# Kernel optimization log

Measured on AMD Instinct MI355X. Metric: run time of the kernel, lower is better.

## Reference

```python
import jax, jax.numpy as jnp
import numpy as np

VOCAB, E, HID, T = 100000, 256, 512, 12
H = HID // 2          # per-direction LSTM hidden
B, S = 64, 256
START, STOP = 10, 11  # tag_to_ix['<START>'], tag_to_ix['<STOP>']
NEG = -10000.0


def setup_inputs() -> dict:
    key = jax.random.key(0)
    ks = jax.random.split(key, 16)
    inp = {
        'batch_sentence': jax.random.randint(ks[0], (B, S), 0, VOCAB),
        'sentence_length': S,
        'batch_chars2': jnp.zeros((1,), jnp.int64 if jax.config.jax_enable_x64 else jnp.int32),
        'chars2_length': 1,
        'emb': jax.random.normal(ks[1], (VOCAB, E), jnp.float32),
        # PyTorch LSTM layout: W_ih [4H, in], W_hh [4H, H], gate order i,f,g,o
        'Wih_f': jax.random.normal(ks[2], (4 * H, E), jnp.float32) * 0.05,
        'Whh_f': jax.random.normal(ks[3], (4 * H, H), jnp.float32) * 0.05,
        'bih_f': jnp.zeros((4 * H,), jnp.float32),
        'bhh_f': jnp.zeros((4 * H,), jnp.float32),
        'Wih_b': jax.random.normal(ks[4], (4 * H, E), jnp.float32) * 0.05,
        'Whh_b': jax.random.normal(ks[5], (4 * H, H), jnp.float32) * 0.05,
        'bih_b': jnp.zeros((4 * H,), jnp.float32),
        'bhh_b': jnp.zeros((4 * H,), jnp.float32),
        'Wt': jax.random.normal(ks[6], (T, HID), jnp.float32) * 0.05,
        'bt': jnp.zeros((T,), jnp.float32),
        'transitions': jax.random.normal(ks[7], (T, T), jnp.float32),
        # init_hidden() draws randn hidden state: h0/c0 [2 dirs, B, H]
        'h0': jax.random.normal(ks[8], (2, B, H), jnp.float32),
        'c0': jax.random.normal(ks[9], (2, B, H), jnp.float32),
    }
    return inp


def _lstm(x, h0, c0, Wih, Whh, bih, bhh):
    # x: [S, B, E] -> hs: [S, B, H]
    def step(carry, xt):
        h, c = carry
        g = xt @ Wih.T + h @ Whh.T + (bih + bhh)
        i, f, gg, o = jnp.split(g, 4, axis=-1)
        c = jax.nn.sigmoid(f) * c + jax.nn.sigmoid(i) * jnp.tanh(gg)
        h = jax.nn.sigmoid(o) * jnp.tanh(c)
        return (h, c), h
    _, hs = jax.lax.scan(step, (h0, c0), x)
    return hs


def _viterbi(feats, transitions):
    # feats: [S, T] emissions for one sequence
    init = jnp.full((T,), NEG, feats.dtype).at[START].set(0.0)

    def step(fv, feat):
        scores = fv[None, :] + transitions            # [next_tag, prev_tag]
        new_fv = jnp.max(scores, axis=1) + feat       # best prev per next
        bptr = jnp.argmax(scores, axis=1)
        return new_fv, bptr

    fv, bptrs = jax.lax.scan(step, init, feats)       # bptrs: [S, T]
    term = fv + transitions[STOP]
    term = term.at[STOP].set(NEG).at[START].set(NEG)  # torch code masks these
    last = jnp.argmax(term)
    score = term[last]

    def back(tag, bptr):
        return bptr[tag], tag                          # y_t = tag at time t
    _, path = jax.lax.scan(back, last, bptrs, reverse=True)
    return score, path


def reference(batch_sentence, sentence_length, batch_chars2, chars2_length,
              emb, Wih_f, Whh_f, bih_f, bhh_f, Wih_b, Whh_b, bih_b, bhh_b,
              Wt, bt, transitions, h0, c0):
    # word embeddings (dropout = identity at inference)
    x = emb[batch_sentence].transpose(1, 0, 2)        # [S, B, E]
    hf = _lstm(x, h0[0], c0[0], Wih_f, Whh_f, bih_f, bhh_f)
    hb = _lstm(x[::-1], h0[1], c0[1], Wih_b, Whh_b, bih_b, bhh_b)[::-1]
    out = jnp.concatenate([hf, hb], axis=-1)          # [S, B, HID]
    feats = out @ Wt.T + bt                           # [S, B, T]
    feats = feats.transpose(1, 0, 2)                  # [B, S, T]
    scores, paths = jax.vmap(_viterbi, in_axes=(0, None))(feats, transitions)
    return scores, paths
```

## Files before the change

kernel.cpp:

```cpp
#include <hip/hip_runtime.h>
#include <cstdint>
#include <cstddef>

#define EDIM 256
#define HID  512
#define NTAG 12
#define HDIM 256
#define BB   64
#define SS   256
#define START_TAG 10
#define STOP_TAG  11
#define NEGV (-10000.0f)
#define NWGD 32
#define UPW  8

typedef __attribute__((ext_vector_type(8))) short bf16x8;
typedef __attribute__((ext_vector_type(4))) float f32x4;

__device__ __forceinline__ unsigned short bf16_rne(float x) {
  union { float f; unsigned u; } a; a.f = x;
  return (unsigned short)((a.u + 0x7fffu + ((a.u >> 16) & 1u)) >> 16);
}
__device__ __forceinline__ float bf16_tof(unsigned short h) {
  union { unsigned u; float f; } a; a.u = ((unsigned)h) << 16; return a.f;
}
__device__ __forceinline__ void unpack8(const unsigned* u, bf16x8& hi, bf16x8& lo) {
#pragma unroll
  for (int j = 0; j < 8; ++j) {
    hi[j] = (short)(u[j] & 0xffffu);
    lo[j] = (short)(u[j] >> 16);
  }
}
__device__ __forceinline__ void pack_hilo(const float* xf, bf16x8& hi, bf16x8& lo) {
#pragma unroll
  for (int j = 0; j < 8; ++j) {
    unsigned short hb = bf16_rne(xf[j]);
    hi[j] = (short)hb;
    lo[j] = (short)bf16_rne(xf[j] - bf16_tof(hb));
  }
}

__global__ void k0_gather(const int* __restrict__ sent,
                          const float* __restrict__ emb,
                          unsigned int* __restrict__ xpk) {
  int t = blockIdx.x;
  for (int n = threadIdx.x; n < BB * EDIM; n += 256) {
    int b = n >> 8, k = n & 255;
    int tok = sent[b * SS + t];
    float x = emb[(size_t)tok * EDIM + k];
    unsigned short hb = bf16_rne(x);
    unsigned short lb = bf16_rne(x - bf16_tof(hb));
    xpk[((size_t)t * BB + b) * EDIM + k] = (unsigned)hb | ((unsigned)lb << 16);
  }
}

__global__ void __launch_bounds__(256)
k1_mfma(const unsigned int* __restrict__ xpk,
        const float* __restrict__ WihF, const float* __restrict__ WihB,
        const float* __restrict__ bihF, const float* __restrict__ bhhF,
        const float* __restrict__ bihB, const float* __restrict__ bhhB,
        float* __restrict__ pre) {
  int blk = blockIdx.x;
  int rg = blk & 15, t = (blk >> 4) & 255, d = blk >> 12;
  const float* Wih = d ? WihB : WihF;
  const float* bi  = d ? bihB : bihF;
  const float* bh2 = d ? bhhB : bhhF;
  int tid = threadIdx.x, lane = tid & 63, v = tid >> 6;
  int l15 = lane & 15, l4 = lane >> 4;

  int Rrow = rg * 64 + v * 16 + l15;
  const float* wrow = Wih + (size_t)Rrow * EDIM;
  bf16x8 Ahi[8], Alo[8];
#pragma unroll
  for (int kk = 0; kk < 8; ++kk) {
    float4 f0 = *(const float4*)(wrow + kk * 32 + l4 * 8);
    float4 f1 = *(const float4*)(wrow + kk * 32 + l4 * 8 + 4);
    float xf[8] = {f0.x, f0.y, f0.z, f0.w, f1.x, f1.y, f1.z, f1.w};
    pack_hilo(xf, Ahi[kk], Alo[kk]);
  }
  float b4[4];
#pragma unroll
  for (int r = 0; r < 4; ++r) {
    int Racc = rg * 64 + v * 16 + l4 * 4 + r;
    b4[r] = bi[Racc] + bh2[Racc];
  }
  const unsigned int* xt = xpk + (size_t)t * BB * EDIM;
  size_t obase = ((size_t)d * SS + t) * 1024 * BB;
#pragma unroll
  for (int ct = 0; ct < 4; ++ct) {
    f32x4 acc = {b4[0], b4[1], b4[2], b4[3]};
    int col = ct * 16 + l15;
    const unsigned int* xc = xt + (size_t)col * EDIM;
#pragma unroll
    for (int kk = 0; kk < 8; ++kk) {
      uint4 q0 = *(const uint4*)(xc + kk * 32 + l4 * 8);
      uint4 q1 = *(const uint4*)(xc + kk * 32 + l4 * 8 + 4);
      unsigned u[8] = {q0.x, q0.y, q0.z, q0.w, q1.x, q1.y, q1.z, q1.w};
      bf16x8 bhf, blf;
      unpack8(u, bhf, blf);
      acc = __builtin_amdgcn_mfma_f32_16x16x32_bf16(Ahi[kk], bhf, acc, 0, 0, 0);
      acc = __builtin_amdgcn_mfma_f32_16x16x32_bf16(Ahi[kk], blf, acc, 0, 0, 0);
      acc = __builtin_amdgcn_mfma_f32_16x16x32_bf16(Alo[kk], bhf, acc, 0, 0, 0);
    }
#pragma unroll
    for (int r = 0; r < 4; ++r) {
      int Racc = rg * 64 + v * 16 + l4 * 4 + r;
      pre[obase + (size_t)Racc * BB + col] = acc[r];
    }
  }
}

__global__ void __launch_bounds__(256, 1)
lstm_mfma(const float* __restrict__ WhhF, const float* __restrict__ WhhB,
          const float* __restrict__ h0, const float* __restrict__ c0,
          const float* __restrict__ pre, float* __restrict__ hseq,
          unsigned int* __restrict__ hx) {
  const int bid = blockIdx.x;
  const int d = bid >> 5, w = bid & 31;
  const int tid = threadIdx.x;
  const int lane = tid & 63;
  const int v = tid >> 6;
  const int l15 = lane & 15, l4 = lane >> 4;
  const int up = tid >> 5;
  const int b2 = (tid & 31) * 2;
  const float* Whh = d ? WhhB : WhhF;

  __shared__ float Cl[32][65];
  __shared__ float cst[UPW][BB];

  bf16x8 Ahi[2][8], Alo[2][8];
#pragma unroll
  for (int rt = 0; rt < 2; ++rt) {
    int i = rt * 16 + l15;
    int R = ((i >> 3) << 8) + w * UPW + (i & 7);
    const float* wrow = Whh + (size_t)R * HDIM;
#pragma unroll
    for (int kk = 0; kk < 8; ++kk) {
      float4 f0 = *(const float4*)(wrow + kk * 32 + l4 * 8);
      float4 f1 = *(const float4*)(wrow + kk * 32 + l4 * 8 + 4);
      float xf[8] = {f0.x, f0.y, f0.z, f0.w, f1.x, f1.y, f1.z, f1.w};
      pack_hilo(xf, Ahi[rt][kk], Alo[rt][kk]);
    }
  }
  cst[up][b2]     = c0[((size_t)d * BB + b2)     * HDIM + (w * UPW + up)];
  cst[up][b2 + 1] = c0[((size_t)d * BB + b2 + 1) * HDIM + (w * UPW + up)];
  __syncthreads();

  const int bcol = v * 16 + l15;
  const int kg = w * UPW + up;

  for (int s = 0; s < SS; ++s) {
    const int t = d ? (SS - 1 - s) : s;

    const float* pbase = pre + (((size_t)d * SS + t) * 1024) * BB + bcol;
    f32x4 acc0, acc1;
#pragma unroll
    for (int r = 0; r < 4; ++r) {
      int i0 = l4 * 4 + r;
      int R0 = ((i0 >> 3) << 8) + w * UPW + (i0 & 7);
      acc0[r] = pbase[(size_t)R0 * BB];
      int i1 = 16 + i0;
      int R1 = ((i1 >> 3) << 8) + w * UPW + (i1 & 7);
      acc1[r] = pbase[(size_t)R1 * BB];
    }

    unsigned uv[64];
    if (s > 0) {
      const unsigned* slot =
          hx + (((size_t)d * 4 + ((s - 1) & 3)) * HDIM) * BB + bcol;
      while (true) {
        int bad = 0;
#pragma unroll
        for (int kk = 0; kk < 8; ++kk)
#pragma unroll
          for (int j = 0; j < 8; ++j) {
            unsigned val = __hip_atomic_load(
                slot + (size_t)(kk * 32 + l4 * 8 + j) * BB,
                __ATOMIC_RELAXED, __HIP_MEMORY_SCOPE_AGENT);
            uv[kk * 8 + j] = val;
            bad |= (val == 0xFFFFFFFFu);
          }
        if (!__any(bad)) break;
        __builtin_amdgcn_s_sleep(1);
      }
      __builtin_amdgcn_sched_barrier(0);
    }

    {
      unsigned long long* ra = (unsigned long long*)(
          hx + (((size_t)d * 4 + ((s + 1) & 3)) * HDIM + kg) * BB + b2);
      __hip_atomic_store(ra, 0xFFFFFFFFFFFFFFFFull,
                         __ATOMIC_RELAXED, __HIP_MEMORY_SCOPE_AGENT);
    }

    if (s == 0) {
      const float* hrow = h0 + ((size_t)d * BB + bcol) * HDIM;
#pragma unroll
      for (int kk = 0; kk < 8; ++kk) {
        float4 f0 = *(const float4*)(hrow + kk * 32 + l4 * 8);
        float4 f1 = *(const float4*)(hrow + kk * 32 + l4 * 8 + 4);
        float xf[8] = {f0.x, f0.y, f0.z, f0.w, f1.x, f1.y, f1.z, f1.w};
        bf16x8 bh, bl;
        pack_hilo(xf, bh, bl);
        acc0 = __builtin_amdgcn_mfma_f32_16x16x32_bf16(Ahi[0][kk], bh, acc0, 0, 0, 0);
        acc0 = __builtin_amdgcn_mfma_f32_16x16x32_bf16(Ahi[0][kk], bl, acc0, 0, 0, 0);
        acc0 = __builtin_amdgcn_mfma_f32_16x16x32_bf16(Alo[0][kk], bh, acc0, 0, 0, 0);
        acc1 = __builtin_amdgcn_mfma_f32_16x16x32_bf16(Ahi[1][kk], bh, acc1, 0, 0, 0);
        acc1 = __builtin_amdgcn_mfma_f32_16x16x32_bf16(Ahi[1][kk], bl, acc1, 0, 0, 0);
        acc1 = __builtin_amdgcn_mfma_f32_16x16x32_bf16(Alo[1][kk], bh, acc1, 0, 0, 0);
      }
    } else {
#pragma unroll
      for (int kk = 0; kk < 8; ++kk) {
        bf16x8 bh, bl;
        unpack8(&uv[kk * 8], bh, bl);
        acc0 = __builtin_amdgcn_mfma_f32_16x16x32_bf16(Ahi[0][kk], bh, acc0, 0, 0, 0);
        acc0 = __builtin_amdgcn_mfma_f32_16x16x32_bf16(Ahi[0][kk], bl, acc0, 0, 0, 0);
        acc0 = __builtin_amdgcn_mfma_f32_16x16x32_bf16(Alo[0][kk], bh, acc0, 0, 0, 0);
        acc1 = __builtin_amdgcn_mfma_f32_16x16x32_bf16(Ahi[1][kk], bh, acc1, 0, 0, 0);
        acc1 = __builtin_amdgcn_mfma_f32_16x16x32_bf16(Ahi[1][kk], bl, acc1, 0, 0, 0);
        acc1 = __builtin_amdgcn_mfma_f32_16x16x32_bf16(Alo[1][kk], bh, acc1, 0, 0, 0);
      }
    }

#pragma unroll
    for (int r = 0; r < 4; ++r) {
      Cl[l4 * 4 + r][bcol] = acc0[r];
      Cl[16 + l4 * 4 + r][bcol] = acc1[r];
    }
    __syncthreads();

    float hn[2]; unsigned pv[2];
#pragma unroll
    for (int e = 0; e < 2; ++e) {
      int b = b2 + e;
      float iv = Cl[up][b], fv = Cl[8 + up][b];
      float gv = Cl[16 + up][b], ov = Cl[24 + up][b];
      float si = 1.f / (1.f + expf(-iv));
      float sf = 1.f / (1.f + expf(-fv));
      float so = 1.f / (1.f + expf(-ov));
      float cn = sf * cst[up][b] + si * tanhf(gv);
      cst[up][b] = cn;
      float h = so * tanhf(cn);
      hn[e] = h;
      unsigned short hb = bf16_rne(h);
      unsigned short lb = bf16_rne(h - bf16_tof(hb));
      pv[e] = (unsigned)hb | ((unsigned)lb << 16);
    }
    *(float2*)&hseq[(((size_t)d * SS + t) * HDIM + kg) * BB + b2] =
        make_float2(hn[0], hn[1]);

    asm volatile("s_waitcnt vmcnt(0)" ::: "memory");

    unsigned long long pv64 =
        (unsigned long long)pv[0] | ((unsigned long long)pv[1] << 32);
    unsigned long long* pd = (unsigned long long*)(
        hx + (((size_t)d * 4 + (s & 3)) * HDIM + kg) * BB + b2);
    __hip_atomic_store(pd, pv64, __ATOMIC_RELAXED, __HIP_MEMORY_SCOPE_AGENT);
  }
}

__global__ void k3_feats(const float* __restrict__ hseq,
                         const float* __restrict__ Wt,
                         const float* __restrict__ bt,
                         float* __restrict__ feats) {
  int t = blockIdx.x, tid = threadIdx.x;
  __shared__ float Wl[NTAG][HID];
  for (int n = tid; n < NTAG * HID; n += 256) Wl[n >> 9][n & 511] = Wt[n];
  __syncthreads();
  int b = tid & 63, tq = tid >> 6;
  float acc[3];
  for (int c = 0; c < 3; ++c) acc[c] = bt[tq * 3 + c];
  const float* hf = hseq + ((size_t)0 * SS + t) * HDIM * BB;
  const float* hb = hseq + ((size_t)1 * SS + t) * HDIM * BB;
  for (int k = 0; k < HDIM; ++k) {
    float h1 = hf[(size_t)k * BB + b];
    float h2 = hb[(size_t)k * BB + b];
#pragma unroll
    for (int c = 0; c < 3; ++c) {
      acc[c] += h1 * Wl[tq * 3 + c][k];
      acc[c] += h2 * Wl[tq * 3 + c][HDIM + k];
    }
  }
  for (int c = 0; c < 3; ++c)
    feats[((size_t)t * BB + b) * NTAG + tq * 3 + c] = acc[c];
}

__global__ void k4_viterbi(const float* __restrict__ feats,
                           const float* __restrict__ trans,
                           float* __restrict__ out) {
  int b = blockIdx.x, lane = threadIdx.x;
  __shared__ float tr[NTAG][NTAG];
  __shared__ float fv[NTAG], fnew[NTAG], term[NTAG];
  __shared__ unsigned char bp[SS][NTAG];
  for (int n = lane; n < NTAG * NTAG; n += 64) tr[n / NTAG][n % NTAG] = trans[n];
  if (lane < NTAG) fv[lane] = (lane == START_TAG) ? 0.f : NEGV;
  __syncthreads();
  for (int s = 0; s < SS; ++s) {
    if (lane < NTAG) {
      float best = fv[0] + tr[lane][0]; int arg = 0;
#pragma unroll
      for (int j = 1; j < NTAG; ++j) {
        float vv = fv[j] + tr[lane][j];
        if (vv > best) { best = vv; arg = j; }
      }
      fnew[lane] = best + feats[((size_t)s * BB + b) * NTAG + lane];
      bp[s][lane] = (unsigned char)arg;
    }
    __syncthreads();
    if (lane < NTAG) fv[lane] = fnew[lane];
    __syncthreads();
  }
  if (lane < NTAG) {
    float vv = fv[lane] + tr[STOP_TAG][lane];
    if (lane == STOP_TAG || lane == START_TAG) vv = NEGV;
    term[lane] = vv;
  }
  __syncthreads();
  if (lane == 0) {
    float best = term[0]; int arg = 0;
    for (int j = 1; j < NTAG; ++j)
      if (term[j] > best) { best = term[j]; arg = j; }
    out[b] = best;
    int cur = arg;
    for (int s = SS - 1; s >= 0; --s) {
      out[64 + (size_t)b * SS + s] = (float)cur;
      cur = bp[s][cur];
    }
  }
}

extern "C" void kernel_launch(void* const* d_in, const int* in_sizes, int n_in,
                              void* d_out, int out_size, void* d_ws, size_t ws_size,
                              hipStream_t stream) {
  (void)in_sizes; (void)n_in; (void)out_size;
  const int*   sent  = (const int*)d_in[0];
  const float* emb   = (const float*)d_in[4];
  const float* WihF  = (const float*)d_in[5];
  const float* WhhF  = (const float*)d_in[6];
  const float* bihF  = (const float*)d_in[7];
  const float* bhhF  = (const float*)d_in[8];
  const float* WihB  = (const float*)d_in[9];
  const float* WhhB  = (const float*)d_in[10];
  const float* bihB  = (const float*)d_in[11];
  const float* bhhB  = (const float*)d_in[12];
  const float* Wt    = (const float*)d_in[13];
  const float* bt    = (const float*)d_in[14];
  const float* trans = (const float*)d_in[15];
  const float* h0    = (const float*)d_in[16];
  const float* c0    = (const float*)d_in[17];
  float* out = (float*)d_out;

  char* ws = (char*)d_ws;
  unsigned int* hx = (unsigned int*)ws;
  float* pre   = (float*)(ws + 524288ull);
  float* hseq  = (float*)(ws + 524288ull + 134217728ull);
  unsigned int* xpk = (unsigned int*)hseq;
  float* feats = (float*)(ws + 524288ull + 134217728ull + 33554432ull);
  if (ws_size < 169082880ull) return;

  hipMemsetAsync(hx, 0xFF, 524288ull, stream);
  k0_gather<<<SS, 256, 0, stream>>>(sent, emb, xpk);
  k1_mfma<<<8192, 256, 0, stream>>>(xpk, WihF, WihB, bihF, bhhF, bihB, bhhB, pre);
  lstm_mfma<<<64, 256, 0, stream>>>(WhhF, WhhB, h0, c0, pre, hseq, hx);
  k3_feats<<<SS, 256, 0, stream>>>(hseq, Wt, bt, feats);
  k4_viterbi<<<BB, 64, 0, stream>>>(feats, trans, out);
}
```

Before: 1.597 ms.

## Remove LDS barrier from LSTM step via lane shuffles and 64-bit h exchange

The recurrent LSTM kernel no longer stages gate pre-activations through shared memory with a __syncthreads each step. Each lane now gets its four gates from its MFMA accumulators plus a cross-half __shfl_xor, and the cell state lives in registers. The hidden-state exchange buffer is relaid out batch-major, so each lane polls with 64-bit atomic loads (32 instead of 64). The three split-precision MFMA chains now use separate accumulators to shorten dependency chains. The hseq store moves after the publish store. Risks are the correctness of the new gate-to-lane mapping and less coalesced hseq writes.

```diff
diff --git a/kernel.cpp b/kernel.cpp
--- a/kernel.cpp
+++ b/kernel.cpp
@@ -11,7 +11,6 @@
 #define START_TAG 10
 #define STOP_TAG  11
 #define NEGV (-10000.0f)
-#define NWGD 32
 #define UPW  8
 
 typedef __attribute__((ext_vector_type(8))) short bf16x8;
@@ -114,19 +113,18 @@
 lstm_mfma(const float* __restrict__ WhhF, const float* __restrict__ WhhB,
           const float* __restrict__ h0, const float* __restrict__ c0,
           const float* __restrict__ pre, float* __restrict__ hseq,
-          unsigned int* __restrict__ hx) {
+          unsigned long long* __restrict__ hx64) {
   const int bid = blockIdx.x;
   const int d = bid >> 5, w = bid & 31;
   const int tid = threadIdx.x;
   const int lane = tid & 63;
   const int v = tid >> 6;
   const int l15 = lane & 15, l4 = lane >> 4;
-  const int up = tid >> 5;
-  const int b2 = (tid & 31) * 2;
+  const int bcol = v * 16 + l15;
+  const int u2 = ((l4 & 1) << 2) | ((l4 >> 1) << 1);
+  const bool low = (l4 < 2);
+  const int kg0 = w * UPW + u2;
   const float* Whh = d ? WhhB : WhhF;
-
-  __shared__ float Cl[32][65];
-  __shared__ float cst[UPW][BB];
 
   bf16x8 Ahi[2][8], Alo[2][8];
 #pragma unroll
@@ -142,43 +140,41 @@
       pack_hilo(xf, Ahi[rt][kk], Alo[rt][kk]);
     }
   }
-  cst[up][b2]     = c0[((size_t)d * BB + b2)     * HDIM + (w * UPW + up)];
-  cst[up][b2 + 1] = c0[((size_t)d * BB + b2 + 1) * HDIM + (w * UPW + up)];
-  __syncthreads();
-
-  const int bcol = v * 16 + l15;
-  const int kg = w * UPW + up;
+  float c2[2];
+  c2[0] = c0[((size_t)d * BB + bcol) * HDIM + kg0];
+  c2[1] = c0[((size_t)d * BB + bcol) * HDIM + kg0 + 1];
 
   for (int s = 0; s < SS; ++s) {
     const int t = d ? (SS - 1 - s) : s;
 
     const float* pbase = pre + (((size_t)d * SS + t) * 1024) * BB + bcol;
-    f32x4 acc0, acc1;
+    f32x4 accA, accD;
 #pragma unroll
     for (int r = 0; r < 4; ++r) {
       int i0 = l4 * 4 + r;
       int R0 = ((i0 >> 3) << 8) + w * UPW + (i0 & 7);
-      acc0[r] = pbase[(size_t)R0 * BB];
+      accA[r] = pbase[(size_t)R0 * BB];
       int i1 = 16 + i0;
       int R1 = ((i1 >> 3) << 8) + w * UPW + (i1 & 7);
-      acc1[r] = pbase[(size_t)R1 * BB];
-    }
-
-    unsigned uv[64];
+      accD[r] = pbase[(size_t)R1 * BB];
+    }
+    f32x4 accB = {0.f, 0.f, 0.f, 0.f}, accC = accB, accE = accB, accF = accB;
+
+    unsigned long long uq[32];
     if (s > 0) {
-      const unsigned* slot =
-          hx + (((size_t)d * 4 + ((s - 1) & 3)) * HDIM) * BB + bcol;
+      const unsigned long long* slot =
+          hx64 + ((size_t)(d * 4 + ((s - 1) & 3)) * BB + bcol) * 128;
       while (true) {
         int bad = 0;
 #pragma unroll
         for (int kk = 0; kk < 8; ++kk)
 #pragma unroll
-          for (int j = 0; j < 8; ++j) {
-            unsigned val = __hip_atomic_load(
-                slot + (size_t)(kk * 32 + l4 * 8 + j) * BB,
+          for (int j2 = 0; j2 < 4; ++j2) {
+            unsigned long long val = __hip_atomic_load(
+                slot + kk * 16 + l4 * 4 + j2,
                 __ATOMIC_RELAXED, __HIP_MEMORY_SCOPE_AGENT);
-            uv[kk * 8 + j] = val;
-            bad |= (val == 0xFFFFFFFFu);
+            uq[kk * 4 + j2] = val;
+            bad |= (val == 0xFFFFFFFFFFFFFFFFull);
           }
         if (!__any(bad)) break;
         __builtin_amdgcn_s_sleep(1);
@@ -186,12 +182,9 @@
       __builtin_amdgcn_sched_barrier(0);
     }
 
-    {
-      unsigned long long* ra = (unsigned long long*)(
-          hx + (((size_t)d * 4 + ((s + 1) & 3)) * HDIM + kg) * BB + b2);
-      __hip_atomic_store(ra, 0xFFFFFFFFFFFFFFFFull,
-                         __ATOMIC_RELAXED, __HIP_MEMORY_SCOPE_AGENT);
-    }
+    __hip_atomic_store(
+        hx64 + ((size_t)(d * 4 + ((s + 1) & 3)) * BB + bcol) * 128 + (kg0 >> 1),
+        0xFFFFFFFFFFFFFFFFull, __ATOMIC_RELAXED, __HIP_MEMORY_SCOPE_AGENT);
 
     if (s == 0) {
       const float* hrow = h0 + ((size_t)d * BB + bcol) * HDIM;
@@ -202,61 +195,71 @@
         float xf[8] = {f0.x, f0.y, f0.z, f0.w, f1.x, f1.y, f1.z, f1.w};
         bf16x8 bh, bl;
         pack_hilo(xf, bh, bl);
-        acc0 = __builtin_amdgcn_mfma_f32_16x16x32_bf16(Ahi[0][kk], bh, acc0, 0, 0, 0);
-        acc0 = __builtin_amdgcn_mfma_f32_16x16x32_bf16(Ahi[0][kk], bl, acc0, 0, 0, 0);
-        acc0 = __builtin_amdgcn_mfma_f32_16x16x32_bf16(Alo[0][kk], bh, acc0, 0, 0, 0);
-        acc1 = __builtin_amdgcn_mfma_f32_16x16x32_bf16(Ahi[1][kk], bh, acc1, 0, 0, 0);
-        acc1 = __builtin_amdgcn_mfma_f32_16x16x32_bf16(Ahi[1][kk], bl, acc1, 0, 0, 0);
-        acc1 = __builtin_amdgcn_mfma_f32_16x16x32_bf16(Alo[1][kk], bh, acc1, 0, 0, 0);
+        accA = __builtin_amdgcn_mfma_f32_16x16x32_bf16(Ahi[0][kk], bh, accA, 0, 0, 0);
+        accB = __builtin_amdgcn_mfma_f32_16x16x32_bf16(Ahi[0][kk], bl, accB, 0, 0, 0);
+        accC = __builtin_amdgcn_mfma_f32_16x16x32_bf16(Alo[0][kk], bh, accC, 0, 0, 0);
+        accD = __builtin_amdgcn_mfma_f32_16x16x32_bf16(Ahi[1][kk], bh, accD, 0, 0, 0);
+        accE = __builtin_amdgcn_mfma_f32_16x16x32_bf16(Ahi[1][kk], bl, accE, 0, 0, 0);
+        accF = __builtin_amdgcn_mfma_f32_16x16x32_bf16(Alo[1][kk], bh, accF, 0, 0, 0);
       }
     } else {
 #pragma unroll
       for (int kk = 0; kk < 8; ++kk) {
+        unsigned long long q0 = uq[kk * 4 + 0], q1 = uq[kk * 4 + 1];
+        unsigned long long q2 = uq[kk * 4 + 2], q3 = uq[kk * 4 + 3];
+        unsigned u[8] = {(unsigned)q0, (unsigned)(q0 >> 32),
+                         (unsigned)q1, (unsigned)(q1 >> 32),
+                         (unsigned)q2, (unsigned)(q2 >> 32),
+                         (unsigned)q3, (unsigned)(q3 >> 32)};
         bf16x8 bh, bl;
-        unpack8(&uv[kk * 8], bh, bl);
-        acc0 = __builtin_amdgcn_mfma_f32_16x16x32_bf16(Ahi[0][kk], bh, acc0, 0, 0, 0);
-        acc0 = __builtin_amdgcn_mfma_f32_16x16x32_bf16(Ahi[0][kk], bl, acc0, 0, 0, 0);
-        acc0 = __builtin_amdgcn_mfma_f32_16x16x32_bf16(Alo[0][kk], bh, acc0, 0, 0, 0);
-        acc1 = __builtin_amdgcn_mfma_f32_16x16x32_bf16(Ahi[1][kk], bh, acc1, 0, 0, 0);
-        acc1 = __builtin_amdgcn_mfma_f32_16x16x32_bf16(Ahi[1][kk], bl, acc1, 0, 0, 0);
-        acc1 = __builtin_amdgcn_mfma_f32_16x16x32_bf16(Alo[1][kk], bh, acc1, 0, 0, 0);
+        unpack8(u, bh, bl);
+        accA = __builtin_amdgcn_mfma_f32_16x16x32_bf16(Ahi[0][kk], bh, accA, 0, 0, 0);
+        accB = __builtin_amdgcn_mfma_f32_16x16x32_bf16(Ahi[0][kk], bl, accB, 0, 0, 0);
+        accC = __builtin_amdgcn_mfma_f32_16x16x32_bf16(Alo[0][kk], bh, accC, 0, 0, 0);
+        accD = __builtin_amdgcn_mfma_f32_16x16x32_bf16(Ahi[1][kk], bh, accD, 0, 0, 0);
+        accE = __builtin_amdgcn_mfma_f32_16x16x32_bf16(Ahi[1][kk], bl, accE, 0, 0, 0);
+        accF = __builtin_amdgcn_mfma_f32_16x16x32_bf16(Alo[1][kk], bh, accF, 0, 0, 0);
       }
     }
-
+    f32x4 acc0 = accA + accB + accC;
+    f32x4 acc1 = accD + accE + accF;
+
+    f32x4 r0, r1;
 #pragma unroll
     for (int r = 0; r < 4; ++r) {
-      Cl[l4 * 4 + r][bcol] = acc0[r];
-      Cl[16 + l4 * 4 + r][bcol] = acc1[r];
-    }
-    __syncthreads();
+      r0[r] = __shfl_xor(acc0[r], 32);
+      r1[r] = __shfl_xor(acc1[r], 32);
+    }
 
     float hn[2]; unsigned pv[2];
 #pragma unroll
     for (int e = 0; e < 2; ++e) {
-      int b = b2 + e;
-      float iv = Cl[up][b], fv = Cl[8 + up][b];
-      float gv = Cl[16 + up][b], ov = Cl[24 + up][b];
+      float iv = low ? acc0[e]     : r0[2 + e];
+      float fv = low ? r0[e]       : acc0[2 + e];
+      float gv = low ? acc1[e]     : r1[2 + e];
+      float ov = low ? r1[e]       : acc1[2 + e];
       float si = 1.f / (1.f + expf(-iv));
       float sf = 1.f / (1.f + expf(-fv));
       float so = 1.f / (1.f + expf(-ov));
-      float cn = sf * cst[up][b] + si * tanhf(gv);
-      cst[up][b] = cn;
+      float cn = sf * c2[e] + si * tanhf(gv);
+      c2[e] = cn;
       float h = so * tanhf(cn);
       hn[e] = h;
       unsigned short hb = bf16_rne(h);
       unsigned short lb = bf16_rne(h - bf16_tof(hb));
       pv[e] = (unsigned)hb | ((unsigned)lb << 16);
     }
-    *(float2*)&hseq[(((size_t)d * SS + t) * HDIM + kg) * BB + b2] =
-        make_float2(hn[0], hn[1]);
 
     asm volatile("s_waitcnt vmcnt(0)" ::: "memory");
 
     unsigned long long pv64 =
         (unsigned long long)pv[0] | ((unsigned long long)pv[1] << 32);
-    unsigned long long* pd = (unsigned long long*)(
-        hx + (((size_t)d * 4 + (s & 3)) * HDIM + kg) * BB + b2);
-    __hip_atomic_store(pd, pv64, __ATOMIC_RELAXED, __HIP_MEMORY_SCOPE_AGENT);
+    __hip_atomic_store(
+        hx64 + ((size_t)(d * 4 + (s & 3)) * BB + bcol) * 128 + (kg0 >> 1),
+        pv64, __ATOMIC_RELAXED, __HIP_MEMORY_SCOPE_AGENT);
+
+    hseq[(((size_t)d * SS + t) * HDIM + kg0) * BB + bcol] = hn[0];
+    hseq[(((size_t)d * SS + t) * HDIM + kg0 + 1) * BB + bcol] = hn[1];
   }
 }
 
@@ -352,17 +355,17 @@
   float* out = (float*)d_out;
 
   char* ws = (char*)d_ws;
-  unsigned int* hx = (unsigned int*)ws;
+  unsigned long long* hx64 = (unsigned long long*)ws;
   float* pre   = (float*)(ws + 524288ull);
   float* hseq  = (float*)(ws + 524288ull + 134217728ull);
   unsigned int* xpk = (unsigned int*)hseq;
   float* feats = (float*)(ws + 524288ull + 134217728ull + 33554432ull);
   if (ws_size < 169082880ull) return;
 
-  hipMemsetAsync(hx, 0xFF, 524288ull, stream);
+  hipMemsetAsync(hx64, 0xFF, 524288ull, stream);
   k0_gather<<<SS, 256, 0, stream>>>(sent, emb, xpk);
   k1_mfma<<<8192, 256, 0, stream>>>(xpk, WihF, WihB, bihF, bhhF, bihB, bhhB, pre);
-  lstm_mfma<<<64, 256, 0, stream>>>(WhhF, WhhB, h0, c0, pre, hseq, hx);
+  lstm_mfma<<<64, 256, 0, stream>>>(WhhF, WhhB, h0, c0, pre, hseq, hx64);
   k3_feats<<<SS, 256, 0, stream>>>(hseq, Wt, bt, feats);
   k4_viterbi<<<BB, 64, 0, stream>>>(feats, trans, out);
 }
```

Measured after the change: 2.560 ms. 60.3% more time.
